# Kernel tuning notes

Hardware: AMD Instinct MI355X
Metric: run time of the kernel (lower is better)

## Reference

```python
import jax, jax.numpy as jnp
import numpy as np


def setup_inputs() -> dict:
    key = jax.random.key(0)
    k1, k2, k3, k4, k5 = jax.random.split(key, 5)
    bs, ns, seq_len = 32, 512, 1024
    n_heads, d_r, d_model = 8, 64, 256
    return {
        "x": jax.random.normal(k1, (bs, ns, seq_len), dtype=jnp.float32),
        "routers": jax.random.normal(k2, (n_heads, d_r, d_model), dtype=jnp.float32),
        "w_kv_weight": jax.random.normal(k3, (n_heads * d_model, seq_len), dtype=jnp.float32) * 0.02,
        "proj_weight": jax.random.normal(k4, (seq_len, n_heads * d_model), dtype=jnp.float32) * 0.02,
        "proj_bias": jax.random.normal(k5, (seq_len,), dtype=jnp.float32) * 0.02,
    }


def reference(x, routers, w_kv_weight, proj_weight, proj_bias):
    # x: (bs, ns, seq_len); routers: (H, d_r, d_model)
    bs, ns, _ = x.shape
    H, d_r, d_model = routers.shape
    qk_scale = 1.0 / jnp.sqrt(jnp.asarray(d_model, x.dtype))
    # shared K=V projection: (bs, ns, H*d_model) -> (bs, H, ns, d_model)
    kv = (x @ w_kv_weight.T).reshape(bs, ns, H, d_model).transpose(0, 2, 1, 3)
    # low-rank learned queries attend over the ns axis: (bs, H, d_r, ns)
    attn_score = jnp.einsum('hrd,bhnd->bhrn', routers, kv) * qk_scale
    attn_weight = jax.nn.softmax(attn_score, axis=-1)
    # dropout is identity in eval/reference mode
    out = jnp.einsum('bhrn,bhnd->bhrd', attn_weight, kv)  # (bs, H, d_r, d_model)
    out = out.transpose(0, 2, 1, 3).reshape(bs, d_r, H * d_model)
    out = out @ proj_weight.T + proj_bias  # (bs, d_r, seq_len)
    return out, attn_weight
```

## Files before the change

### kernel.cpp

```cpp
#include <hip/hip_runtime.h>
#include <hip/hip_bf16.h>


typedef __attribute__((ext_vector_type(8))) short short8;
typedef __attribute__((ext_vector_type(4))) float f32x4;
typedef __attribute__((ext_vector_type(4))) unsigned int uint4v;
typedef __attribute__((ext_vector_type(4))) unsigned short ushort4v;

__device__ inline unsigned short f2bf(float f) {
  unsigned int u = __float_as_uint(f);
  u += 0x7FFFu + ((u >> 16) & 1u);
  return (unsigned short)(u >> 16);
}

__device__ __forceinline__ void async_copy16(unsigned short* lds, const unsigned short* g) {
  __builtin_amdgcn_global_load_lds(
      (const __attribute__((address_space(1))) unsigned int*)g,
      (__attribute__((address_space(3))) unsigned int*)lds,
      16, 0, 0);
}

__global__ __launch_bounds__(256) void cast_all(
    const float* __restrict__ x, const float* __restrict__ wkv, const float* __restrict__ projw,
    unsigned short* __restrict__ xb, unsigned short* __restrict__ wkv_b,
    unsigned short* __restrict__ projw_b, float* __restrict__ out0) {
  int i = blockIdx.x * 256 + threadIdx.x;
  if (i >= 5242880) {
    ((float4*)out0)[i - 5242880] = float4{0.f, 0.f, 0.f, 0.f};
    return;
  }
  const float* src; unsigned short* dst; int off;
  if (i < 524288)        { src = wkv;   dst = wkv_b;   off = i; }
  else if (i < 1048576)  { src = projw; dst = projw_b; off = i - 524288; }
  else                   { src = x;     dst = xb;      off = i - 1048576; }
  float4 v = ((const float4*)src)[off];
  ushort4v w; w.x = f2bf(v.x); w.y = f2bf(v.y); w.z = f2bf(v.z); w.w = f2bf(v.w);
  ((ushort4v*)dst)[off] = w;
}

__global__ __launch_bounds__(512, 1) void gemm1_8phase(
    const unsigned short* __restrict__ A, const unsigned short* __restrict__ B,
    unsigned short* __restrict__ C, int lda, int ldb, int ldc, int K, int nWGn)
{
  __shared__ __align__(16) unsigned short sA[2][2][8192];
  __shared__ __align__(16) unsigned short sB[2][2][8192];

  const int tid = threadIdx.x;
  const int cpx = gridDim.x >> 3;
  const int swz = (blockIdx.x & 7) * cpx + (blockIdx.x >> 3);
  const int bn = swz % nWGn, bm = swz / nWGn;

  const int wave = tid >> 6, lane = tid & 63;
  const int wm = wave >> 2, wn = wave & 3;
  const int lr = lane & 15, ls = lane >> 4;
  const int lsw8 = (ls ^ ((lr >> 1) & 3)) * 8;

  const int r0 = tid >> 2;
  const int sl0 = (tid & 3) ^ ((tid >> 3) & 3);
  const unsigned short* gA = A + (long long)(bm * 256 + r0) * lda + sl0 * 8;
  const unsigned short* gB = B + (long long)(bn * 256 + r0) * ldb + sl0 * 8;
  const long long lda128 = (long long)128 * lda, ldb128 = (long long)128 * ldb;

#define STA(b_, k_, t_) { const unsigned short* g_ = gA + (t_) * 64 + (k_) * 32; \
    async_copy16(&sA[b_][k_][tid * 8], g_); \
    async_copy16(&sA[b_][k_][4096 + tid * 8], g_ + lda128); }
#define STB(b_, k_, t_) { const unsigned short* g_ = gB + (t_) * 64 + (k_) * 32; \
    async_copy16(&sB[b_][k_][tid * 8], g_); \
    async_copy16(&sB[b_][k_][4096 + tid * 8], g_ + ldb128); }

  f32x4 acc[8][4];
  #pragma unroll
  for (int mi = 0; mi < 8; ++mi)
    #pragma unroll
    for (int ni = 0; ni < 4; ++ni)
      acc[mi][ni] = f32x4{0.f, 0.f, 0.f, 0.f};

  const int KT = K >> 6;
  STB(0, 0, 0) STA(0, 0, 0) STB(0, 1, 0) STA(0, 1, 0)
  if (KT > 1) {
    STB(1, 0, 1) STA(1, 0, 1) STB(1, 1, 1)
    asm volatile("s_waitcnt vmcnt(6)" ::: "memory");
  } else {
    asm volatile("s_waitcnt vmcnt(0)" ::: "memory");
  }
  __builtin_amdgcn_s_barrier();
  __builtin_amdgcn_sched_barrier(0);

  for (int t = 0; t < KT; ++t) {
    const int b = t & 1, nb = b ^ 1;
    const bool hasT1 = (t + 1) < KT, hasT2 = (t + 2) < KT;
    short8 af[4], bf[4];

    #pragma unroll
    for (int mi = 0; mi < 4; ++mi)
      af[mi] = *(const short8*)&sA[b][0][(wm * 128 + mi * 16 + lr) * 32 + lsw8];
    #pragma unroll
    for (int ni = 0; ni < 4; ++ni)
      bf[ni] = *(const short8*)&sB[b][0][(wn * 64 + ni * 16 + lr) * 32 + lsw8];
    if (hasT1) { STA(nb, 1, t + 1) }
    __builtin_amdgcn_s_setprio(1);
    #pragma unroll
    for (int mi = 0; mi < 4; ++mi)
      #pragma unroll
      for (int ni = 0; ni < 4; ++ni)
        acc[mi][ni] = __builtin_amdgcn_mfma_f32_16x16x32_bf16(af[mi], bf[ni], acc[mi][ni], 0, 0, 0);
    __builtin_amdgcn_s_setprio(0);
    __builtin_amdgcn_s_barrier();

    #pragma unroll
    for (int mi = 0; mi < 4; ++mi)
      af[mi] = *(const short8*)&sA[b][0][(wm * 128 + (4 + mi) * 16 + lr) * 32 + lsw8];
    if (hasT2) { STB(b, 0, t + 2) }
    __builtin_amdgcn_s_setprio(1);
    #pragma unroll
    for (int mi = 0; mi < 4; ++mi)
      #pragma unroll
      for (int ni = 0; ni < 4; ++ni)
        acc[4 + mi][ni] = __builtin_amdgcn_mfma_f32_16x16x32_bf16(af[mi], bf[ni], acc[4 + mi][ni], 0, 0, 0);
    __builtin_amdgcn_s_setprio(0);
    __builtin_amdgcn_s_barrier();

    #pragma unroll
    for (int mi = 0; mi < 4; ++mi)
      af[mi] = *(const short8*)&sA[b][1][(wm * 128 + mi * 16 + lr) * 32 + lsw8];
    #pragma unroll
    for (int ni = 0; ni < 4; ++ni)
      bf[ni] = *(const short8*)&sB[b][1][(wn * 64 + ni * 16 + lr) * 32 + lsw8];
    if (hasT2) { STA(b, 0, t + 2) }
    __builtin_amdgcn_s_setprio(1);
    #pragma unroll
    for (int mi = 0; mi < 4; ++mi)
      #pragma unroll
      for (int ni = 0; ni < 4; ++ni)
        acc[mi][ni] = __builtin_amdgcn_mfma_f32_16x16x32_bf16(af[mi], bf[ni], acc[mi][ni], 0, 0, 0);
    __builtin_amdgcn_s_setprio(0);
    __builtin_amdgcn_s_barrier();

    #pragma unroll
    for (int mi = 0; mi < 4; ++mi)
      af[mi] = *(const short8*)&sA[b][1][(wm * 128 + (4 + mi) * 16 + lr) * 32 + lsw8];
    if (hasT2) { STB(b, 1, t + 2) }
    __builtin_amdgcn_s_setprio(1);
    #pragma unroll
    for (int mi = 0; mi < 4; ++mi)
      #pragma unroll
      for (int ni = 0; ni < 4; ++ni)
        acc[4 + mi][ni] = __builtin_amdgcn_mfma_f32_16x16x32_bf16(af[mi], bf[ni], acc[4 + mi][ni], 0, 0, 0);
    __builtin_amdgcn_s_setprio(0);
    if (t == KT - 2) {
      asm volatile("s_waitcnt vmcnt(0)" ::: "memory");
    } else if (t < KT - 2) {
      asm volatile("s_waitcnt vmcnt(6)" ::: "memory");
    }
    __builtin_amdgcn_s_barrier();
    __builtin_amdgcn_sched_barrier(0);
  }
#undef STA
#undef STB

  #pragma unroll
  for (int mi = 0; mi < 8; ++mi) {
    #pragma unroll
    for (int ni = 0; ni < 4; ++ni) {
      int row = bm * 256 + wm * 128 + mi * 16 + ls * 4;
      int col = bn * 256 + wn * 64 + ni * 16 + lr;
      #pragma unroll
      for (int r = 0; r < 4; ++r)
        C[(long long)(row + r) * ldc + col] = f2bf(acc[mi][ni][r]);
    }
  }
}

__global__ __launch_bounds__(1024, 1) void score_softmax_pv(
    const float* __restrict__ routers,
    const unsigned short* __restrict__ kv,
    float* __restrict__ attnw,
    unsigned short* __restrict__ ao)
{
  __shared__ __align__(16) char smem[151552];
  unsigned short* lds_a = (unsigned short*)smem;
  unsigned short* lds_b = (unsigned short*)(smem + 9216);
  unsigned short* P_lds = (unsigned short*)(smem + 9216);
  unsigned short* kvT   = (unsigned short*)(smem + 82944);
  float* redmax = (float*)(smem + 149504);
  float* redsum = (float*)(smem + 150528);

  const int bh = blockIdx.x;
  const int b = bh >> 3, h = bh & 7;
  const int tid = threadIdx.x;
  const int wave = tid >> 6, lane = tid & 63;
  const int wm = wave >> 2, wn = wave & 3;
  const int lr = lane & 15, ls = lane >> 4;
  const int lk = ls * 8;

  const unsigned short* kvb = kv + (long long)b * 512 * 2048 + h * 256;
  const float* Rh = routers + h * 16384;

#define STAGE_KVT(dt_) { _Pragma("unroll") \
    for (int i = 0; i < 4; ++i) { \
      int c = i * 1024 + tid; \
      int n = c & 511, dgrp = c >> 9; \
      uint4v v = *(const uint4v*)&kvb[(long long)n * 2048 + (dt_) * 64 + dgrp * 8]; \
      const unsigned short* pv = (const unsigned short*)&v; \
      _Pragma("unroll") \
      for (int j = 0; j < 8; ++j) kvT[(dgrp * 8 + j) * 520 + n] = pv[j]; \
    } }

  f32x4 acc[8];
  #pragma unroll
  for (int ni = 0; ni < 8; ++ni) acc[ni] = f32x4{0.f, 0.f, 0.f, 0.f};

  for (int k0 = 0; k0 < 256; k0 += 64) {
    {
      int r = tid >> 4, kc = (tid & 15) * 4;
      float4 v = *(const float4*)(Rh + r * 256 + k0 + kc);
      ushort4v w; w.x = f2bf(v.x); w.y = f2bf(v.y); w.z = f2bf(v.z); w.w = f2bf(v.w);
      *(ushort4v*)&lds_a[r * 72 + kc] = w;
    }
    #pragma unroll
    for (int i = 0; i < 4; ++i) {
      int c = i * 1024 + tid;
      int r = c >> 3, kc = (c & 7) * 8;
      *(uint4v*)&lds_b[r * 72 + kc] = *(const uint4v*)(kvb + (long long)r * 2048 + k0 + kc);
    }
    __syncthreads();
    #pragma unroll
    for (int kk = 0; kk < 2; ++kk) {
      short8 af = *(const short8*)&lds_a[(wm * 16 + lr) * 72 + kk * 32 + lk];
      #pragma unroll
      for (int ni = 0; ni < 8; ++ni) {
        short8 bf = *(const short8*)&lds_b[(wn * 128 + ni * 16 + lr) * 72 + kk * 32 + lk];
        acc[ni] = __builtin_amdgcn_mfma_f32_16x16x32_bf16(af, bf, acc[ni], 0, 0, 0);
      }
    }
    __syncthreads();
  }

  STAGE_KVT(0)

  #pragma unroll
  for (int q = 0; q < 4; ++q) {
    int row = wm * 16 + ls * 4 + q;
    float m = -1e30f;
    #pragma unroll
    for (int ni = 0; ni < 8; ++ni) { acc[ni][q] *= 0.0625f; m = fmaxf(m, acc[ni][q]); }
    #pragma unroll
    for (int d = 1; d < 16; d <<= 1) m = fmaxf(m, __shfl_xor(m, d, 64));
    if (lr == 0) redmax[row * 4 + wn] = m;
  }
  __syncthreads();
  #pragma unroll
  for (int q = 0; q < 4; ++q) {
    int row = wm * 16 + ls * 4 + q;
    float M = fmaxf(fmaxf(redmax[row * 4 + 0], redmax[row * 4 + 1]),
                    fmaxf(redmax[row * 4 + 2], redmax[row * 4 + 3]));
    float s = 0.f;
    #pragma unroll
    for (int ni = 0; ni < 8; ++ni) { float p = __expf(acc[ni][q] - M); acc[ni][q] = p; s += p; }
    #pragma unroll
    for (int d = 1; d < 16; d <<= 1) s += __shfl_xor(s, d, 64);
    if (lr == 0) redsum[row * 4 + wn] = s;
  }
  __syncthreads();
  #pragma unroll
  for (int q = 0; q < 4; ++q) {
    int row = wm * 16 + ls * 4 + q;
    float inv = 1.0f / (redsum[row * 4 + 0] + redsum[row * 4 + 1] +
                        redsum[row * 4 + 2] + redsum[row * 4 + 3]);
    long long base = (long long)bh * 32768 + row * 512 + wn * 128;
    #pragma unroll
    for (int ni = 0; ni < 8; ++ni) {
      float wv = acc[ni][q] * inv;
      attnw[base + ni * 16 + lr] = wv;
      P_lds[row * 520 + wn * 128 + ni * 16 + lr] = f2bf(wv);
    }
  }

  for (int dt = 0; dt < 4; ++dt) {
    if (dt != 0) { STAGE_KVT(dt) }
    __syncthreads();
    f32x4 accp = f32x4{0.f, 0.f, 0.f, 0.f};
    #pragma unroll
    for (int kk = 0; kk < 16; ++kk) {
      short8 af = *(const short8*)&P_lds[(wm * 16 + lr) * 520 + kk * 32 + lk];
      short8 bf = *(const short8*)&kvT[(wn * 16 + lr) * 520 + kk * 32 + lk];
      accp = __builtin_amdgcn_mfma_f32_16x16x32_bf16(af, bf, accp, 0, 0, 0);
    }
    #pragma unroll
    for (int q = 0; q < 4; ++q) {
      int r = wm * 16 + ls * 4 + q;
      ao[(long long)(b * 64 + r) * 2048 + h * 256 + dt * 64 + wn * 16 + lr] = f2bf(accp[q]);
    }
    __syncthreads();
  }
#undef STAGE_KVT
}

template<int BM,int BN,int BK,int WM,int WN,bool DO_BIAS>
__global__ __launch_bounds__(256) void gemm_bt_splitk(
    const unsigned short* __restrict__ Ap, const unsigned short* __restrict__ Bp,
    float* __restrict__ Cv, const float* __restrict__ bias,
    int lda, int ldb, int ldc, int Kslice, int nWGn)
{
  constexpr int STRA = BK + 8;
  constexpr int STRB = BK + 8;
  constexpr int NWN = BN / WN;
  constexpr int MF = WM / 16, NF = WN / 16;
  __shared__ __align__(16) unsigned short lds_a[BM * STRA];
  __shared__ __align__(16) unsigned short lds_b[BN * STRB];

  const int tid = threadIdx.x;
  const int bn = blockIdx.x % nWGn;
  const int bm = blockIdx.x / nWGn;
  const int kp = blockIdx.y;

  const int wave = tid >> 6, lane = tid & 63;
  const int wm = wave / NWN, wn = wave % NWN;
  const int lr = lane & 15;
  const int lk = (lane >> 4) * 8;

  const long long abase = (long long)bm * BM * lda + (long long)kp * Kslice;
  const long long bbase = (long long)bn * BN * ldb + (long long)kp * Kslice;

  f32x4 acc[MF][NF];
  #pragma unroll
  for (int mi = 0; mi < MF; ++mi)
    #pragma unroll
    for (int ni = 0; ni < NF; ++ni)
      acc[mi][ni] = f32x4{0.f, 0.f, 0.f, 0.f};

  for (int k0 = 0; k0 < Kslice; k0 += BK) {
    {
      const unsigned short* Ab2 = Ap + abase + k0;
      #pragma unroll
      for (int i = 0; i < BM*BK/2048; ++i) {
        int c = i*256 + tid;
        int r = c / (BK/8);
        int kc = (c % (BK/8)) * 8;
        *(uint4v*)&lds_a[r*STRA + kc] = *(const uint4v*)(Ab2 + (long long)r*lda + kc);
      }
    }
    {
      const unsigned short* Bb2 = Bp + bbase + k0;
      #pragma unroll
      for (int i = 0; i < BN*BK/2048; ++i) {
        int c = i*256 + tid;
        int r = c / (BK/8);
        int kc = (c % (BK/8)) * 8;
        *(uint4v*)&lds_b[r*STRB + kc] = *(const uint4v*)(Bb2 + (long long)r*ldb + kc);
      }
    }
    __syncthreads();

    #pragma unroll
    for (int kk = 0; kk < BK/32; ++kk) {
      short8 af[MF]; short8 bfr[NF];
      #pragma unroll
      for (int mi = 0; mi < MF; ++mi)
        af[mi] = *(const short8*)&lds_a[(wm*WM + mi*16 + lr)*STRA + kk*32 + lk];
      #pragma unroll
      for (int ni = 0; ni < NF; ++ni)
        bfr[ni] = *(const short8*)&lds_b[(wn*WN + ni*16 + lr)*STRB + kk*32 + lk];
      #pragma unroll
      for (int mi = 0; mi < MF; ++mi)
        #pragma unroll
        for (int ni = 0; ni < NF; ++ni)
          acc[mi][ni] = __builtin_amdgcn_mfma_f32_16x16x32_bf16(af[mi], bfr[ni], acc[mi][ni], 0, 0, 0);
    }
    __syncthreads();
  }

  const int cr0 = (lane >> 4) * 4;
  #pragma unroll
  for (int mi = 0; mi < MF; ++mi) {
    #pragma unroll
    for (int ni = 0; ni < NF; ++ni) {
      int row = bm*BM + wm*WM + mi*16 + cr0;
      int col = bn*BN + wn*WN + ni*16 + lr;
      float badd = (DO_BIAS && kp == 0) ? bias[col] : 0.f;
      #pragma unroll
      for (int r = 0; r < 4; ++r) {
        float x = acc[mi][ni][r] + badd;
        unsafeAtomicAdd(&Cv[(long long)(row + r) * ldc + col], x);
      }
    }
  }
}

extern "C" void kernel_launch(void* const* d_in, const int* in_sizes, int n_in,
                              void* d_out, int out_size, void* d_ws, size_t ws_size,
                              hipStream_t stream) {
  const float* x       = (const float*)d_in[0];
  const float* routers = (const float*)d_in[1];
  const float* wkv     = (const float*)d_in[2];
  const float* projw   = (const float*)d_in[3];
  const float* pbias   = (const float*)d_in[4];

  char* ws = (char*)d_ws;
  unsigned short* wkv_b   = (unsigned short*)(ws);
  unsigned short* projw_b = (unsigned short*)(ws +  4194304);
  unsigned short* kv_b    = (unsigned short*)(ws +  8388608);
  unsigned short* xb      = (unsigned short*)(ws + 75497472);
  unsigned short* ao_b    = (unsigned short*)(ws + 92536832);

  float* out0  = (float*)d_out;
  float* attnw = out0 + 2097152;

  cast_all<<<22528, 256, 0, stream>>>(x, wkv, projw, xb, wkv_b, projw_b, out0);

  gemm1_8phase<<<512, 512, 0, stream>>>(xb, wkv_b, kv_b, 1024, 1024, 2048, 1024, 8);

  score_softmax_pv<<<256, 1024, 0, stream>>>(routers, kv_b, attnw, ao_b);

  gemm_bt_splitk<64,128,64,64,32,true><<<dim3(256,2), 256, 0, stream>>>(
      ao_b, projw_b, out0, pbias, 2048, 2048, 1024, 1024, 8);
}
```

Before: 160.5 us.

## Rewrite projection GEMM with direct global-to-LDS loads and larger tiles

Replaces the templated split-K projection GEMM with a dedicated kernel that stages A and B tiles straight into LDS using global_load_lds async copies instead of going through registers. The tile grows from 64x128 to 128x128, each wave computes a 64x64 sub-tile, and split-K rises from 2 to 4 slices. The aim is fewer register round-trips and better operand reuse in the final GEMM. In exchange the unpadded LDS layout may cause bank conflicts, and the extra K slices double the atomic adds into the output.

```diff
diff --git a/kernel.cpp b/kernel.cpp
--- a/kernel.cpp
+++ b/kernel.cpp
@@ -296,18 +296,13 @@
 #undef STAGE_KVT
 }
 
-template<int BM,int BN,int BK,int WM,int WN,bool DO_BIAS>
-__global__ __launch_bounds__(256) void gemm_bt_splitk(
-    const unsigned short* __restrict__ Ap, const unsigned short* __restrict__ Bp,
-    float* __restrict__ Cv, const float* __restrict__ bias,
+__global__ __launch_bounds__(256) void proj_glds_splitk(
+    const unsigned short* __restrict__ A, const unsigned short* __restrict__ B,
+    float* __restrict__ C, const float* __restrict__ bias,
     int lda, int ldb, int ldc, int Kslice, int nWGn)
 {
-  constexpr int STRA = BK + 8;
-  constexpr int STRB = BK + 8;
-  constexpr int NWN = BN / WN;
-  constexpr int MF = WM / 16, NF = WN / 16;
-  __shared__ __align__(16) unsigned short lds_a[BM * STRA];
-  __shared__ __align__(16) unsigned short lds_b[BN * STRB];
+  __shared__ __align__(16) unsigned short sA[128 * 64];
+  __shared__ __align__(16) unsigned short sB[128 * 64];
 
   const int tid = threadIdx.x;
   const int bn = blockIdx.x % nWGn;
@@ -315,56 +310,45 @@
   const int kp = blockIdx.y;
 
   const int wave = tid >> 6, lane = tid & 63;
-  const int wm = wave / NWN, wn = wave % NWN;
+  const int wm = wave >> 1, wn = wave & 1;
   const int lr = lane & 15;
   const int lk = (lane >> 4) * 8;
 
-  const long long abase = (long long)bm * BM * lda + (long long)kp * Kslice;
-  const long long bbase = (long long)bn * BN * ldb + (long long)kp * Kslice;
-
-  f32x4 acc[MF][NF];
-  #pragma unroll
-  for (int mi = 0; mi < MF; ++mi)
-    #pragma unroll
-    for (int ni = 0; ni < NF; ++ni)
+  const unsigned short* Ab = A + (long long)(bm * 128 + (tid >> 3)) * lda + (tid & 7) * 8
+                               + (long long)kp * Kslice;
+  const unsigned short* Bb = B + (long long)(bn * 128 + (tid >> 3)) * ldb + (tid & 7) * 8
+                               + (long long)kp * Kslice;
+  unsigned short* sAp = &sA[tid * 8];
+  unsigned short* sBp = &sB[tid * 8];
+
+  f32x4 acc[4][4];
+  #pragma unroll
+  for (int mi = 0; mi < 4; ++mi)
+    #pragma unroll
+    for (int ni = 0; ni < 4; ++ni)
       acc[mi][ni] = f32x4{0.f, 0.f, 0.f, 0.f};
 
-  for (int k0 = 0; k0 < Kslice; k0 += BK) {
-    {
-      const unsigned short* Ab2 = Ap + abase + k0;
-      #pragma unroll
-      for (int i = 0; i < BM*BK/2048; ++i) {
-        int c = i*256 + tid;
-        int r = c / (BK/8);
-        int kc = (c % (BK/8)) * 8;
-        *(uint4v*)&lds_a[r*STRA + kc] = *(const uint4v*)(Ab2 + (long long)r*lda + kc);
-      }
-    }
-    {
-      const unsigned short* Bb2 = Bp + bbase + k0;
-      #pragma unroll
-      for (int i = 0; i < BN*BK/2048; ++i) {
-        int c = i*256 + tid;
-        int r = c / (BK/8);
-        int kc = (c % (BK/8)) * 8;
-        *(uint4v*)&lds_b[r*STRB + kc] = *(const uint4v*)(Bb2 + (long long)r*ldb + kc);
-      }
-    }
-    __syncthreads();
-
-    #pragma unroll
-    for (int kk = 0; kk < BK/32; ++kk) {
-      short8 af[MF]; short8 bfr[NF];
-      #pragma unroll
-      for (int mi = 0; mi < MF; ++mi)
-        af[mi] = *(const short8*)&lds_a[(wm*WM + mi*16 + lr)*STRA + kk*32 + lk];
-      #pragma unroll
-      for (int ni = 0; ni < NF; ++ni)
-        bfr[ni] = *(const short8*)&lds_b[(wn*WN + ni*16 + lr)*STRB + kk*32 + lk];
-      #pragma unroll
-      for (int mi = 0; mi < MF; ++mi)
+  for (int k0 = 0; k0 < Kslice; k0 += 64) {
+    #pragma unroll
+    for (int i = 0; i < 4; ++i) {
+      async_copy16(sAp + i * 2048, Ab + (long long)i * 32 * lda + k0);
+      async_copy16(sBp + i * 2048, Bb + (long long)i * 32 * ldb + k0);
+    }
+    __syncthreads();
+
+    #pragma unroll
+    for (int kk = 0; kk < 2; ++kk) {
+      short8 af[4], bfr[4];
+      #pragma unroll
+      for (int mi = 0; mi < 4; ++mi)
+        af[mi] = *(const short8*)&sA[(wm * 64 + mi * 16 + lr) * 64 + kk * 32 + lk];
+      #pragma unroll
+      for (int ni = 0; ni < 4; ++ni)
+        bfr[ni] = *(const short8*)&sB[(wn * 64 + ni * 16 + lr) * 64 + kk * 32 + lk];
+      #pragma unroll
+      for (int mi = 0; mi < 4; ++mi)
         #pragma unroll
-        for (int ni = 0; ni < NF; ++ni)
+        for (int ni = 0; ni < 4; ++ni)
           acc[mi][ni] = __builtin_amdgcn_mfma_f32_16x16x32_bf16(af[mi], bfr[ni], acc[mi][ni], 0, 0, 0);
     }
     __syncthreads();
@@ -372,17 +356,15 @@
 
   const int cr0 = (lane >> 4) * 4;
   #pragma unroll
-  for (int mi = 0; mi < MF; ++mi) {
-    #pragma unroll
-    for (int ni = 0; ni < NF; ++ni) {
-      int row = bm*BM + wm*WM + mi*16 + cr0;
-      int col = bn*BN + wn*WN + ni*16 + lr;
-      float badd = (DO_BIAS && kp == 0) ? bias[col] : 0.f;
-      #pragma unroll
-      for (int r = 0; r < 4; ++r) {
-        float x = acc[mi][ni][r] + badd;
-        unsafeAtomicAdd(&Cv[(long long)(row + r) * ldc + col], x);
-      }
+  for (int mi = 0; mi < 4; ++mi) {
+    #pragma unroll
+    for (int ni = 0; ni < 4; ++ni) {
+      int row = bm * 128 + wm * 64 + mi * 16 + cr0;
+      int col = bn * 128 + wn * 64 + ni * 16 + lr;
+      float badd = (kp == 0) ? bias[col] : 0.f;
+      #pragma unroll
+      for (int r = 0; r < 4; ++r)
+        unsafeAtomicAdd(&C[(long long)(row + r) * ldc + col], acc[mi][ni][r] + badd);
     }
   }
 }
@@ -412,6 +394,6 @@
 
   score_softmax_pv<<<256, 1024, 0, stream>>>(routers, kv_b, attnw, ao_b);
 
-  gemm_bt_splitk<64,128,64,64,32,true><<<dim3(256,2), 256, 0, stream>>>(
-      ao_b, projw_b, out0, pbias, 2048, 2048, 1024, 1024, 8);
-}
+  proj_glds_splitk<<<dim3(128, 4), 256, 0, stream>>>(
+      ao_b, projw_b, out0, pbias, 2048, 2048, 1024, 512, 8);
+}
```

Result: slower. 169.7 us (+5.7%).
